# Kernel tuning notes

Measured on AMD Instinct MI355X. Metric: run time of the kernel, lower is better.

Reference implementation:

```python
import jax, jax.numpy as jnp
import numpy as np

N = 50000
E = 800000
F_IN = 128
HID = 16
HEADS = 8
C = 16
NEG_SLOPE = 0.2


def setup_inputs() -> dict:
    key = jax.random.key(0)
    ks = jax.random.split(key, 12)
    glorot = lambda k, shape: jax.random.normal(k, shape, jnp.float32) * jnp.sqrt(2.0 / (shape[0] + shape[-1]))
    return {
        "x": jax.random.normal(ks[0], (N, F_IN), jnp.float32),
        "edge_index": jax.random.randint(ks[1], (2, E), 0, N, jnp.int32),
        "x2": jax.random.normal(ks[2], (N, F_IN), jnp.float32),
        "edge_index2": jax.random.randint(ks[3], (2, E), 0, N, jnp.int32),
        # conv1: GATConv(F_IN -> HID, heads=HEADS, concat=True)
        "W1": glorot(ks[4], (F_IN, HEADS * HID)),
        "a1_src": glorot(ks[5], (HEADS, HID)),
        "a1_dst": glorot(ks[6], (HEADS, HID)),
        "b1": jnp.zeros((HEADS * HID,), jnp.float32),
        # conv2: GATConv(HEADS*HID -> C, heads=1, concat=False)
        "W2": glorot(ks[7], (HEADS * HID, 1 * C)),
        "a2_src": glorot(ks[8], (1, C)),
        "a2_dst": glorot(ks[9], (1, C)),
        "b2": jnp.zeros((C,), jnp.float32),
    }


def gat_conv(x, edge_index, W, a_src, a_dst, bias, concat):
    """PyG-style GATConv with self-loops, segment softmax over destinations."""
    n = x.shape[0]
    heads, out = a_src.shape
    h = (x @ W).reshape(n, heads, out)               # [N, H, O]
    loops = jnp.arange(n, dtype=edge_index.dtype)
    src = jnp.concatenate([edge_index[0], loops])     # messages flow src -> dst
    dst = jnp.concatenate([edge_index[1], loops])
    alpha_s = jnp.einsum('nho,ho->nh', h, a_src)
    alpha_d = jnp.einsum('nho,ho->nh', h, a_dst)
    e = jax.nn.leaky_relu(alpha_s[src] + alpha_d[dst], NEG_SLOPE)  # [E+N, H]
    m = jax.lax.stop_gradient(jax.ops.segment_max(e, dst, num_segments=n))
    w = jnp.exp(e - m[dst])
    denom = jax.ops.segment_sum(w, dst, num_segments=n)
    alpha = w / (denom[dst] + 1e-16)                  # segment softmax
    msg = h[src] * alpha[:, :, None]                  # [E+N, H, O]
    agg = jax.ops.segment_sum(msg, dst, num_segments=n)
    agg = agg.reshape(n, heads * out) if concat else agg.mean(axis=1)
    return agg + bias


def forward_once(x, edge_index, W1, a1_src, a1_dst, b1, W2, a2_src, a2_dst, b2):
    # dropout(p=0.6) is identity in eval mode
    h = jax.nn.elu(gat_conv(x, edge_index, W1, a1_src, a1_dst, b1, concat=True))
    return gat_conv(h, edge_index, W2, a2_src, a2_dst, b2, concat=False)


def reference(x, edge_index, x2, edge_index2, W1, a1_src, a1_dst, b1, W2, a2_src, a2_dst, b2):
    y = forward_once(x, edge_index, W1, a1_src, a1_dst, b1, W2, a2_src, a2_dst, b2)
    z = forward_once(x2, edge_index2, W1, a1_src, a1_dst, b1, W2, a2_src, a2_dst, b2)
    eps = 1e-8
    ny = jnp.maximum(jnp.linalg.norm(y, axis=1), eps)
    nz = jnp.maximum(jnp.linalg.norm(z, axis=1), eps)
    cos = jnp.sum(y * z, axis=1) / (ny * nz)
    ls_y = jax.nn.log_softmax(y, axis=1)
    ls_z = jax.nn.log_softmax(z, axis=1)
    return (ls_y, 1.0 - cos, ls_z, ls_y, ls_y)
```

## Files before the change

### kernel.cpp

```cpp
#include <hip/hip_runtime.h>
#include <hip/hip_bf16.h>

#define N_NODES 50000
#define N_EDGES 800000
#define F_INS   128
#define HIDDEN  16
#define HEADS   8
#define HO      128
#define C_OUT   16
#define NEG_SLOPE 0.2f
#define SLOT    64
#define NB_G1   ((N_NODES + 63) / 64)
#define NB_GAT1 ((N_NODES + 3) / 4)

#define NP      50016
#define AS_ST   ((size_t)NP * 8)
#define H1B_ST  ((size_t)NP * 64)
#define H2_ST   ((size_t)NP * 16)
#define AS2_ST  ((size_t)NP)

#define NCLS     128
#define CLS_MUL  1342u
#define CLS_SH   19
#define CAP      8192
#define CHUNK    2048
#define NB_BKT   ((N_EDGES + CHUNK - 1) / CHUNK)
#define GPAD     16

typedef unsigned short u16;
typedef unsigned int   u32;
typedef int v4i __attribute__((ext_vector_type(4)));
typedef short bf16x8 __attribute__((ext_vector_type(8)));
typedef float f32x4 __attribute__((ext_vector_type(4)));

__device__ __forceinline__ float bf2f(u16 u) {
    union { u32 i; float f; } t; t.i = ((u32)u) << 16; return t.f;
}
__device__ __forceinline__ float bflo(u32 q) {
    union { u32 i; float f; } t; t.i = q << 16; return t.f;
}
__device__ __forceinline__ float bfhi(u32 q) {
    union { u32 i; float f; } t; t.i = q & 0xFFFF0000u; return t.f;
}
__device__ __forceinline__ u32 f2bf(float f) {
    union { float f; u32 i; } t; t.f = f;
    u32 x = t.i;
    u32 lsb = (x >> 16) & 1u;
    x += 0x7FFFu + lsb;
    return x >> 16;
}
__device__ __forceinline__ u32 cvtpk(float lo, float hi) {
    u32 r;
    asm("v_cvt_pk_bf16_f32 %0, %1, %2" : "=v"(r) : "v"(lo), "v"(hi));
    return r;
}
__device__ __forceinline__ float lrelu(float t) {
    return fmaxf(t, NEG_SLOPE * t);
}
__device__ __forceinline__ int cls_of(int d) { return (int)(((u32)d * CLS_MUL) >> CLS_SH); }
__host__ __device__ __forceinline__ int cls_base(int c) { return (int)(((u32)c * 524288u + (CLS_MUL - 1)) / CLS_MUL); }

__global__ void k_wt(const float* __restrict__ W1, const float* __restrict__ a1s,
                     const float* __restrict__ a1d, const float* __restrict__ W2,
                     u32* __restrict__ w1t, u32* __restrict__ a1t,
                     float* __restrict__ w2p, int* __restrict__ gcur) {
    int t = threadIdx.x;
    if (blockIdx.x < 32) {
        int e = blockIdx.x * 256 + t;
        int c = e >> 6, kp = e & 63;
        float lo = W1[(2 * kp) * 128 + c];
        float hi = W1[(2 * kp + 1) * 128 + c];
        w1t[e] = (f2bf(hi) << 16) | f2bf(lo);
    } else {
        #pragma unroll
        for (int i = 0; i < GPAD; ++i) gcur[t * GPAD + i] = 0;
        #pragma unroll
        for (int i = 0; i < 8; ++i) {
            int idx = t * 8 + i;
            int f4 = idx >> 2, j = idx & 3;
            int sl = f4 >> 6, lane = f4 & 63;
            int s = (lane >> 4) * 8 + sl, cc = lane & 15;
            w2p[idx] = W2[(4 * s + j) * 16 + cc];
        }
        #pragma unroll
        for (int i = 0; i < 4; ++i) {
            int wi = t + i * 256;
            int n = wi >> 6, kp = wi & 63;
            int h = n >> 1;
            const float* av = ((n & 1) ? a1d : a1s) + h * 16;
            float s0 = 0.f, s1 = 0.f;
            #pragma unroll
            for (int c = 0; c < 16; ++c) {
                s0 += W1[(2 * kp) * 128 + h * 16 + c] * av[c];
                s1 += W1[(2 * kp + 1) * 128 + h * 16 + c] * av[c];
            }
            a1t[wi] = (f2bf(s1) << 16) | f2bf(s0);
        }
    }
}

__launch_bounds__(256)
__global__ void k_bg1(const int* __restrict__ ei0, const int* __restrict__ ei1,
                      int* __restrict__ gcur, u32* __restrict__ bucket,
                      const float* __restrict__ x1g, const float* __restrict__ x2g,
                      const u32* __restrict__ w1t, const u32* __restrict__ a1t,
                      u32* __restrict__ h1b, float* __restrict__ as_,
                      float* __restrict__ ad_) {
    __shared__ int cnt[NCLS];
    __shared__ int bse[NCLS];
    int t = threadIdx.x;

    if (blockIdx.x < 2 * NB_BKT) {
        int g = blockIdx.x & 1;
        int chunk = blockIdx.x >> 1;
        int e0 = chunk * CHUNK + t * 8;
        bool act = e0 < N_EDGES;

        if (t < NCLS) cnt[t] = 0;
        __syncthreads();

        const int* src = g ? ei1 : ei0;
        const int* dst = src + N_EDGES;
        int d8[8], s8[8], c8[8];
        if (act) {
            v4i da = *(const v4i*)(dst + e0), db = *(const v4i*)(dst + e0 + 4);
            v4i sa = *(const v4i*)(src + e0), sb = *(const v4i*)(src + e0 + 4);
            d8[0]=da[0]; d8[1]=da[1]; d8[2]=da[2]; d8[3]=da[3];
            d8[4]=db[0]; d8[5]=db[1]; d8[6]=db[2]; d8[7]=db[3];
            s8[0]=sa[0]; s8[1]=sa[1]; s8[2]=sa[2]; s8[3]=sa[3];
            s8[4]=sb[0]; s8[5]=sb[1]; s8[6]=sb[2]; s8[7]=sb[3];
            #pragma unroll
            for (int j = 0; j < 8; ++j) {
                c8[j] = cls_of(d8[j]);
                atomicAdd(&cnt[c8[j]], 1);
            }
        }
        __syncthreads();
        if (t < NCLS) {
            int n = cnt[t];
            bse[t] = n ? atomicAdd(&gcur[(g * NCLS + t) * GPAD], n) : 0;
            cnt[t] = 0;
        }
        __syncthreads();
        if (act) {
            #pragma unroll
            for (int j = 0; j < 8; ++j) {
                int c = c8[j];
                int p = atomicAdd(&cnt[c], 1);
                bucket[(size_t)(g * NCLS + c) * CAP + bse[c] + p] =
                    ((u32)d8[j] << 16) | (u32)s8[j];
            }
        }
        return;
    }

    int bid = blockIdx.x - 2 * NB_BKT;
    int g = bid >= NB_G1;
    if (g) bid -= NB_G1;
    const float* x = g ? x2g : x1g;
    u32*   h1o = h1b + (size_t)g * H1B_ST;
    float* aso = as_ + (size_t)g * AS_ST;
    float* ado = ad_ + (size_t)g * AS_ST;
    int r0 = bid * 64;

    int lane = t & 63;
    int wid = t >> 6;
    int n = lane & 15, quad = lane >> 4;

    int r = r0 + wid * 16 + n;
    bool rok = r < N_NODES;
    const float4* xr = (const float4*)(x + (size_t)r * 128);
    float4 xf[8];
    #pragma unroll
    for (int kt = 0; kt < 4; ++kt) {
        int cb = kt * 8 + quad * 2;
        xf[kt * 2]     = rok ? xr[cb]     : make_float4(0.f, 0.f, 0.f, 0.f);
        xf[kt * 2 + 1] = rok ? xr[cb + 1] : make_float4(0.f, 0.f, 0.f, 0.f);
    }

    f32x4 acc[8], acca;
    #pragma unroll
    for (int ct = 0; ct < 8; ++ct) acc[ct] = (f32x4){0.f, 0.f, 0.f, 0.f};
    acca = (f32x4){0.f, 0.f, 0.f, 0.f};

    #pragma unroll
    for (int kt = 0; kt < 4; ++kt) {
        union { uint4 u; bf16x8 v; } af;
        float4 f0 = xf[kt * 2], f1 = xf[kt * 2 + 1];
        af.u.x = cvtpk(f0.x, f0.y);
        af.u.y = cvtpk(f0.z, f0.w);
        af.u.z = cvtpk(f1.x, f1.y);
        af.u.w = cvtpk(f1.z, f1.w);
        #pragma unroll
        for (int ct = 0; ct < 8; ++ct) {
            union { uint4 u; bf16x8 v; } bf_;
            bf_.u = *(const uint4*)(w1t + (ct * 16 + n) * 64 + kt * 16 + quad * 4);
            acc[ct] = __builtin_amdgcn_mfma_f32_16x16x32_bf16(af.v, bf_.v, acc[ct], 0, 0, 0);
        }
        union { uint4 u; bf16x8 v; } ba;
        ba.u = *(const uint4*)(a1t + n * 64 + kt * 16 + quad * 4);
        acca = __builtin_amdgcn_mfma_f32_16x16x32_bf16(af.v, ba.v, acca, 0, 0, 0);
    }

    int h = n >> 1;
    #pragma unroll
    for (int reg = 0; reg < 4; ++reg) {
        int gr = r0 + wid * 16 + quad * 4 + reg;
        bool ok = gr <= N_NODES;
        float av = (gr == N_NODES) ? -1e30f : acca[reg];
        if (ok) {
            if (n & 1) ado[gr * 8 + h] = av;
            else       aso[gr * 8 + h] = av;
        }
        #pragma unroll
        for (int ct = 0; ct < 8; ++ct) {
            float ot = __shfl_xor(acc[ct][reg], 1);
            if (!(n & 1) && ok)
                h1o[(size_t)gr * 64 + ct * 8 + (n >> 1)] = cvtpk(acc[ct][reg], ot);
        }
    }
}

__launch_bounds__(1024)
__global__ void k_build(const int* __restrict__ gcur, const u32* __restrict__ bucket,
                        int* __restrict__ cursor, u16* __restrict__ col) {
    __shared__ int cnt[391];
    __shared__ __align__(16) u16 scol[391 * SLOT];
    int t = threadIdx.x;
    int c = blockIdx.x & (NCLS - 1);
    int g = blockIdx.x >> 7;
    int d0 = cls_base(c);
    int d1 = (c == NCLS - 1) ? N_NODES : cls_base(c + 1);
    int nn = d1 - d0;
    for (int j = t; j < nn; j += 1024) cnt[j] = 0;
    __syncthreads();

    int size = gcur[(g * NCLS + c) * GPAD];
    const u32* bp = bucket + (size_t)(g * NCLS + c) * CAP;
    for (int i = t; i < size; i += 1024) {
        u32 e = bp[i];
        int d = (int)(e >> 16);
        int s = (int)(e & 0xFFFFu);
        int p = atomicAdd(&cnt[d - d0], 1);
        if (p < SLOT) scol[(d - d0) * SLOT + p] = (u16)s;
    }
    __syncthreads();
    int* cur = cursor + g * N_NODES;
    for (int j = t; j < nn; j += 1024) {
        int raw = cnt[j];
        int n0 = min(raw, SLOT);
        int n1 = (n0 + 7) & ~7;
        for (int p = n0; p < n1; ++p) scol[j * SLOT + p] = (u16)N_NODES;
        cur[d0 + j] = raw;
    }
    __syncthreads();
    uint4* dst = (uint4*)(col + ((size_t)g * N_NODES + d0) * SLOT);
    const uint4* srcv = (const uint4*)scol;
    int n16 = nn * 8;
    for (int i = t; i < n16; i += 1024) dst[i] = srcv[i];
}

#define GAT1_ISSUE(I, qa0,qb0,qa1,qb1,qa2,qb2,qa3,qb3, A) do { \
    u32 c0_=(I).x, c1_=(I).y, c2_=(I).z, c3_=(I).w; \
    u32 i0_ = usel ? (c0_ >> 16) : (c0_ & 0xFFFFu); \
    u32 i1_ = usel ? (c1_ >> 16) : (c1_ & 0xFFFFu); \
    u32 i2_ = usel ? (c2_ >> 16) : (c2_ & 0xFFFFu); \
    u32 i3_ = usel ? (c3_ >> 16) : (c3_ & 0xFFFFu); \
    uint2 p0_ = *(const uint2*)(h1c + ((i0_ << 8) | l8)); qa0 = p0_.x; qb0 = p0_.y; \
    uint2 p1_ = *(const uint2*)(h1c + ((i1_ << 8) | l8)); qa1 = p1_.x; qb1 = p1_.y; \
    uint2 p2_ = *(const uint2*)(h1c + ((i2_ << 8) | l8)); qa2 = p2_.x; qb2 = p2_.y; \
    uint2 p3_ = *(const uint2*)(h1c + ((i3_ << 8) | l8)); qa3 = p3_.x; qb3 = p3_.y; \
    u32 ds_ = (j8 & 4) ? ((j8 & 2) ? c3_ : c2_) : ((j8 & 2) ? c1_ : c0_); \
    u32 sA_ = (j8 & 1) ? (ds_ >> 16) : (ds_ & 0xFFFFu); \
    A = *(const float*)(asc + ((sA_ << 5) | ha4)); \
} while (0)

#define GAT1_CONS(qa0,qb0,qa1,qb1,qa2,qb2,qa3,qb3, A) do { \
    int wli_ = __float_as_int(__expf(lrelu((A) + ad_a))); \
    float w0 = __int_as_float(__builtin_amdgcn_ds_bpermute(vbn,       wli_)); \
    float w1 = __int_as_float(__builtin_amdgcn_ds_bpermute(vbn + 64,  wli_)); \
    float w2 = __int_as_float(__builtin_amdgcn_ds_bpermute(vbn + 128, wli_)); \
    float w3 = __int_as_float(__builtin_amdgcn_ds_bpermute(vbn + 192, wli_)); \
    denom += ((w0 + w1) + (w2 + w3)); \
    ax0 += w0 * bflo(qa0) + w1 * bflo(qa1) + w2 * bflo(qa2) + w3 * bflo(qa3); \
    ax1 += w0 * bfhi(qa0) + w1 * bfhi(qa1) + w2 * bfhi(qa2) + w3 * bfhi(qa3); \
    ax2 += w0 * bflo(qb0) + w1 * bflo(qb1) + w2 * bflo(qb2) + w3 * bflo(qb3); \
    ax3 += w0 * bfhi(qb0) + w1 * bfhi(qb1) + w2 * bfhi(qb2) + w3 * bfhi(qb3); \
} while (0)

__launch_bounds__(256)
__global__ void k_gat1f(const u32* __restrict__ h1b, const float* __restrict__ as_,
                        const float* __restrict__ ad_, const int* __restrict__ cursor,
                        const u16* __restrict__ col, const float* __restrict__ b1,
                        const float* __restrict__ w2p, const float* __restrict__ a2s,
                        const float* __restrict__ a2d, float* __restrict__ h2,
                        float* __restrict__ as2, float* __restrict__ ad2) {
    int t = threadIdx.x;
    int lane = t & 63;
    int bid = blockIdx.x;
    if (bid == 2 * NB_GAT1) {
        if (t < 32) {
            int g = t >> 4, c = t & 15;
            h2[(size_t)g * H2_ST + (size_t)N_NODES * 16 + c] = 0.f;
            if (c == 0) {
                as2[(size_t)g * AS2_ST + N_NODES] = -1e30f;
                ad2[(size_t)g * AS2_ST + N_NODES] = 0.f;
            }
        }
        return;
    }
    int g = bid >= NB_GAT1;
    if (g) bid -= NB_GAT1;
    int node = bid * 4 + (t >> 6);

    const char*  h1c = (const char*)(h1b + (size_t)g * H1B_ST);
    const char*  asc = (const char*)(as_ + (size_t)g * AS_ST);
    const float* ad1 = ad_ + (size_t)g * AS_ST;
    const u16*   cp  = col + ((size_t)g * N_NODES + node) * SLOT;
    float* h2o  = h2  + (size_t)g * H2_ST;
    float* as2o = as2 + (size_t)g * AS2_ST;
    float* ad2o = ad2 + (size_t)g * AS2_ST;

    int l = lane & 31;
    int usel = lane >> 5;
    u32 l8 = (u32)l << 3;
    int hc = l >> 2;
    int ha = lane & 7;
    int j8 = lane >> 3;
    u32 ha4 = (u32)ha << 2;
    int vbn = usel * 32 + hc * 4;

    float ad_a = ad1[node * 8 + ha];
    float as_c = as_[(size_t)g * AS_ST + node * 8 + hc];
    float ad_c = ad1[node * 8 + hc];

    float w = __expf(lrelu(as_c + ad_c));
    float ws = usel ? 0.f : w;
    uint2 sq = *(const uint2*)(h1c + (((u32)node << 8) | l8));
    float denom = ws;
    float ax0 = ws * bflo(sq.x), ax1 = ws * bfhi(sq.x);
    float ax2 = ws * bflo(sq.y), ax3 = ws * bfhi(sq.y);

    int deg = min(cursor[g * N_NODES + node], SLOT);
    int nb = (deg + 7) >> 3;
    if (nb) {
        u32 a0,b0,a1,b1_,a2,b2,a3,b3;
        u32 c0,d0,c1,d1,c2,d2,c3,d3;
        float Aa, Ab;
        uint4 Ia, Ib;
        Ia = *(const uint4*)cp;
        GAT1_ISSUE(Ia, a0,b0,a1,b1_,a2,b2,a3,b3, Aa);
        if (nb > 1) {
            Ib = *(const uint4*)(cp + 8);
            GAT1_ISSUE(Ib, c0,d0,c1,d1,c2,d2,c3,d3, Ab);
        }
        int b = 0;
        for (;;) {
            GAT1_CONS(a0,b0,a1,b1_,a2,b2,a3,b3, Aa);
            if (++b >= nb) break;
            if (b + 1 < nb) {
                Ia = *(const uint4*)(cp + (b + 1) * 8);
                GAT1_ISSUE(Ia, a0,b0,a1,b1_,a2,b2,a3,b3, Aa);
            }
            GAT1_CONS(c0,d0,c1,d1,c2,d2,c3,d3, Ab);
            if (++b >= nb) break;
            if (b + 1 < nb) {
                Ib = *(const uint4*)(cp + (b + 1) * 8);
                GAT1_ISSUE(Ib, c0,d0,c1,d1,c2,d2,c3,d3, Ab);
            }
        }
    }
    denom += __shfl_xor(denom, 32);
    ax0 += __shfl_xor(ax0, 32);
    ax1 += __shfl_xor(ax1, 32);
    ax2 += __shfl_xor(ax2, 32);
    ax3 += __shfl_xor(ax3, 32);

    float inv = 1.f / (denom + 1e-16f);
    int cb = l * 4;
    float o0 = ax0 * inv + b1[cb];
    float o1 = ax1 * inv + b1[cb + 1];
    float o2 = ax2 * inv + b1[cb + 2];
    float o3 = ax3 * inv + b1[cb + 3];
    o0 = (o0 > 0.f) ? o0 : (__expf(o0) - 1.f);
    o1 = (o1 > 0.f) ? o1 : (__expf(o1) - 1.f);
    o2 = (o2 > 0.f) ? o2 : (__expf(o2) - 1.f);
    o3 = (o3 > 0.f) ? o3 : (__expf(o3) - 1.f);
    u32 q2a = cvtpk(o0, o1);
    u32 q2b = cvtpk(o2, o3);

    int cc = lane & 15, seg = lane >> 4;
    const float4* wr = (const float4*)w2p;
    float acc2 = 0.f;
    #pragma unroll
    for (int sl = 0; sl < 8; ++sl) {
        float4 wv = wr[sl * 64 + lane];
        int sb = (seg * 8 + sl) << 2;
        u32 va = (u32)__builtin_amdgcn_ds_bpermute(sb, (int)q2a);
        u32 vb = (u32)__builtin_amdgcn_ds_bpermute(sb, (int)q2b);
        acc2 += bflo(va) * wv.x + bfhi(va) * wv.y
              + bflo(vb) * wv.z + bfhi(vb) * wv.w;
    }
    acc2 += __shfl_xor(acc2, 16);
    acc2 += __shfl_xor(acc2, 32);
    if (lane < 16) h2o[(u32)node * 16 + cc] = acc2;

    float sa = acc2 * a2s[cc];
    float sd = acc2 * a2d[cc];
    #pragma unroll
    for (int m = 1; m < 16; m <<= 1) {
        sa += __shfl_xor(sa, m);
        sd += __shfl_xor(sd, m);
    }
    if (lane == 0) { as2o[node] = sa; ad2o[node] = sd; }
}

#define G2_ISSUE(I, H2C, ASC, v0,v1,v2,v3,v4,v5,v6,v7, A) do { \
    u32 ix_=(I).x, iy_=(I).y, iz_=(I).z, iw_=(I).w; \
    v0 = *(const float*)((H2C) + (((ix_ & 0xFFFFu) << 6) | c4)); \
    v1 = *(const float*)((H2C) + (((ix_ >> 16)     << 6) | c4)); \
    v2 = *(const float*)((H2C) + (((iy_ & 0xFFFFu) << 6) | c4)); \
    v3 = *(const float*)((H2C) + (((iy_ >> 16)     << 6) | c4)); \
    v4 = *(const float*)((H2C) + (((iz_ & 0xFFFFu) << 6) | c4)); \
    v5 = *(const float*)((H2C) + (((iz_ >> 16)     << 6) | c4)); \
    v6 = *(const float*)((H2C) + (((iw_ & 0xFFFFu) << 6) | c4)); \
    v7 = *(const float*)((H2C) + (((iw_ >> 16)     << 6) | c4)); \
    u32 ds_ = (jsel & 4) ? ((jsel & 2) ? iw_ : iz_) : ((jsel & 2) ? iy_ : ix_); \
    u32 sA_ = (jsel & 1) ? (ds_ >> 16) : (ds_ & 0xFFFFu); \
    A = *(const float*)((ASC) + (sA_ << 2)); \
} while (0)

#define G2_CONS(v0,v1,v2,v3,v4,v5,v6,v7, A, AD, DEN, ACC) do { \
    int wli_ = __float_as_int(__expf(lrelu((A) + (AD)))); \
    float w0 = __int_as_float(__builtin_amdgcn_ds_bpermute(gb,      wli_)); \
    float w1 = __int_as_float(__builtin_amdgcn_ds_bpermute(gb + 4,  wli_)); \
    float w2 = __int_as_float(__builtin_amdgcn_ds_bpermute(gb + 8,  wli_)); \
    float w3 = __int_as_float(__builtin_amdgcn_ds_bpermute(gb + 12, wli_)); \
    float w4 = __int_as_float(__builtin_amdgcn_ds_bpermute(gb + 16, wli_)); \
    float w5 = __int_as_float(__builtin_amdgcn_ds_bpermute(gb + 20, wli_)); \
    float w6 = __int_as_float(__builtin_amdgcn_ds_bpermute(gb + 24, wli_)); \
    float w7 = __int_as_float(__builtin_amdgcn_ds_bpermute(gb + 28, wli_)); \
    DEN += ((w0 + w1) + (w2 + w3)) + ((w4 + w5) + (w6 + w7)); \
    ACC += (w0 * v0 + w1 * v1 + w2 * v2 + w3 * v3) \
         + (w4 * v4 + w5 * v5 + w6 * v6 + w7 * v7); \
} while (0)

__launch_bounds__(256)
__global__ void k_gat2e(const float* __restrict__ h2, const float* __restrict__ as2,
                        const float* __restrict__ ad2, const int* __restrict__ cursor,
                        const u16* __restrict__ col, const float* __restrict__ b2,
                        float* __restrict__ out) {
    int t = threadIdx.x;
    int node = blockIdx.x * 16 + (t >> 4);
    int c = t & 15;
    int lane = t & 63;
    u32 c4 = (u32)c << 2;
    int jsel = lane & 7;
    u32 gb = (u32)(lane & 48) << 2;
    float b2c = b2[c];

    const char* h2Y = (const char*)h2;
    const char* h2Z = (const char*)(h2 + H2_ST);
    const char* asY = (const char*)as2;
    const char* asZ = (const char*)(as2 + AS2_ST);
    const u16* cpY = col + (size_t)node * SLOT;
    const u16* cpZ = col + ((size_t)N_NODES + node) * SLOT;
    float adY = ad2[node];
    float adZ = ad2[AS2_ST + node];

    float wY = __expf(lrelu(*(const float*)(asY + ((u32)node << 2)) + adY));
    float dY = wY;
    float aY = wY * *(const float*)(h2Y + (((u32)node << 6) | c4));
    float wZ = __expf(lrelu(*(const float*)(asZ + ((u32)node << 2)) + adZ));
    float dZ = wZ;
    float aZ = wZ * *(const float*)(h2Z + (((u32)node << 6) | c4));

    int nbY = (min(cursor[node], SLOT) + 7) >> 3;
    int nbZ = (min(cursor[N_NODES + node], SLOT) + 7) >> 3;

    float y0,y1,y2,y3,y4,y5,y6,y7, Ay;
    float z0,z1,z2,z3,z4,z5,z6,z7, Az;
    uint4 I;
    if (nbY) { I = *(const uint4*)cpY; G2_ISSUE(I, h2Y, asY, y0,y1,y2,y3,y4,y5,y6,y7, Ay); }
    if (nbZ) { I = *(const uint4*)cpZ; G2_ISSUE(I, h2Z, asZ, z0,z1,z2,z3,z4,z5,z6,z7, Az); }
    int bY = 0, bZ = 0;
    while (bY < nbY || bZ < nbZ) {
        if (bY < nbY) {
            G2_CONS(y0,y1,y2,y3,y4,y5,y6,y7, Ay, adY, dY, aY);
            ++bY;
            if (bY < nbY) {
                I = *(const uint4*)(cpY + bY * 8);
                G2_ISSUE(I, h2Y, asY, y0,y1,y2,y3,y4,y5,y6,y7, Ay);
            }
        }
        if (bZ < nbZ) {
            G2_CONS(z0,z1,z2,z3,z4,z5,z6,z7, Az, adZ, dZ, aZ);
            ++bZ;
            if (bZ < nbZ) {
                I = *(const uint4*)(cpZ + bZ * 8);
                G2_ISSUE(I, h2Z, asZ, z0,z1,z2,z3,z4,z5,z6,z7, Az);
            }
        }
    }
    float yv = aY / (dY + 1e-16f) + b2c;
    float zv = aZ / (dZ + 1e-16f) + b2c;

    float my = yv, mz = zv;
    #pragma unroll
    for (int m = 1; m < 16; m <<= 1) {
        my = fmaxf(my, __shfl_xor(my, m));
        mz = fmaxf(mz, __shfl_xor(mz, m));
    }
    float sy = __expf(yv - my), sz = __expf(zv - mz);
    float dot = yv * zv, ny = yv * yv, nz = zv * zv;
    #pragma unroll
    for (int m = 1; m < 16; m <<= 1) {
        sy  += __shfl_xor(sy, m);
        sz  += __shfl_xor(sz, m);
        dot += __shfl_xor(dot, m);
        ny  += __shfl_xor(ny, m);
        nz  += __shfl_xor(nz, m);
    }
    float lsey = my + __logf(sy);
    float lsez = mz + __logf(sz);
    float omc = 1.f - dot / (fmaxf(sqrtf(ny), 1e-8f) * fmaxf(sqrtf(nz), 1e-8f));

    const int O1 = N_NODES * C_OUT;
    const int O2 = O1 + N_NODES;
    const int O3 = O2 + N_NODES * C_OUT;
    const int O4 = O3 + N_NODES * C_OUT;
    float ly = yv - lsey;
    float lz = zv - lsez;
    int base = node * 16 + c;
    out[base]      = ly;
    out[O2 + base] = lz;
    out[O3 + base] = ly;
    out[O4 + base] = ly;
    if (c == 0) out[O1 + node] = omc;
}

extern "C" void kernel_launch(void* const* d_in, const int* in_sizes, int n_in,
                              void* d_out, int out_size, void* d_ws, size_t ws_size,
                              hipStream_t stream) {
    (void)in_sizes; (void)n_in; (void)out_size; (void)ws_size;
    const float* x1  = (const float*)d_in[0];
    const int*   ei1 = (const int*)d_in[1];
    const float* x2  = (const float*)d_in[2];
    const int*   ei2 = (const int*)d_in[3];
    const float* W1  = (const float*)d_in[4];
    const float* a1s = (const float*)d_in[5];
    const float* a1d = (const float*)d_in[6];
    const float* b1  = (const float*)d_in[7];
    const float* W2  = (const float*)d_in[8];
    const float* a2s = (const float*)d_in[9];
    const float* a2d = (const float*)d_in[10];
    const float* b2  = (const float*)d_in[11];
    float* out = (float*)d_out;

    char* p = (char*)d_ws;
    int* gcur      = (int*)p; p += (size_t)2 * NCLS * GPAD * 4;
    u32* w1t       = (u32*)p; p += (size_t)128 * 64 * 4;
    u32* a1t       = (u32*)p; p += (size_t)16 * 64 * 4;
    float* w2p     = (float*)p; p += (size_t)16 * 128 * 4;
    int* cursor    = (int*)p; p += (size_t)2 * N_NODES * 4;
    u16* col       = (u16*)p; p += (size_t)2 * N_NODES * SLOT * 2;
    float* as1  = (float*)p; p += (size_t)2 * AS_ST * 4;
    float* ad1  = (float*)p; p += (size_t)2 * AS_ST * 4;
    float* h2   = (float*)p; p += (size_t)2 * H2_ST * 4;
    float* as2  = (float*)p; p += (size_t)2 * AS2_ST * 4;
    float* ad2  = (float*)p; p += (size_t)2 * AS2_ST * 4;
    u32* bucket = (u32*)p;   p += (size_t)2 * NCLS * CAP * 4;
    u32* h1b    = (u32*)p;   p += (size_t)2 * H1B_ST * 4;

    k_wt    <<<33, 256, 0, stream>>>(W1, a1s, a1d, W2, w1t, a1t, w2p, gcur);
    k_bg1   <<<2 * NB_BKT + 2 * NB_G1, 256, 0, stream>>>(ei1, ei2, gcur, bucket,
                                                         x1, x2, w1t, a1t, h1b, as1, ad1);
    k_build <<<2 * NCLS, 1024, 0, stream>>>(gcur, bucket, cursor, col);
    k_gat1f <<<2 * NB_GAT1 + 1, 256, 0, stream>>>(h1b, as1, ad1, cursor, col, b1,
                                                  w2p, a2s, a2d, h2, as2, ad2);
    k_gat2e <<<N_NODES / 16, 256, 0, stream>>>(h2, as2, ad2, cursor, col, b2, out);
}
```

Before: 279.5 us.

## Process two nodes per wavefront in GAT layer-1 with cross-node gather prefetch

Each wavefront in the fused layer-1 aggregation kernel now handles two consecutive destination nodes instead of one, halving the grid size. The first gather batches for the second node are issued before the first node's W2 projection and reductions, so those loads can overlap that epilogue math. This targets exposed gather latency and per-wave setup overhead, at the cost of higher register pressure and less parallelism, which may reduce occupancy.

```diff
diff --git a/kernel.cpp b/kernel.cpp
--- a/kernel.cpp
+++ b/kernel.cpp
@@ -11,7 +11,7 @@
 #define NEG_SLOPE 0.2f
 #define SLOT    64
 #define NB_G1   ((N_NODES + 63) / 64)
-#define NB_GAT1 ((N_NODES + 3) / 4)
+#define NB_GAT1P ((N_NODES + 7) / 8)
 
 #define NP      50016
 #define AS_ST   ((size_t)NP * 8)
@@ -288,6 +288,24 @@
     ax3 += w0 * bfhi(qb0) + w1 * bfhi(qb1) + w2 * bfhi(qb2) + w3 * bfhi(qb3); \
 } while (0)
 
+#define GAT1_LOOP(CP, NB) do { \
+    int b_ = 0; \
+    for (;;) { \
+        GAT1_CONS(a0,b0,a1,b1_,a2,b2,a3,b3, Aa); \
+        if (++b_ >= (NB)) break; \
+        if (b_ + 1 < (NB)) { \
+            I4 = *(const uint4*)((CP) + (b_ + 1) * 8); \
+            GAT1_ISSUE(I4, a0,b0,a1,b1_,a2,b2,a3,b3, Aa); \
+        } \
+        GAT1_CONS(c0,d0,c1,d1,c2,d2,c3,d3, Ab); \
+        if (++b_ >= (NB)) break; \
+        if (b_ + 1 < (NB)) { \
+            I4 = *(const uint4*)((CP) + (b_ + 1) * 8); \
+            GAT1_ISSUE(I4, c0,d0,c1,d1,c2,d2,c3,d3, Ab); \
+        } \
+    } \
+} while (0)
+
 __launch_bounds__(256)
 __global__ void k_gat1f(const u32* __restrict__ h1b, const float* __restrict__ as_,
                         const float* __restrict__ ad_, const int* __restrict__ cursor,
@@ -298,7 +316,7 @@
     int t = threadIdx.x;
     int lane = t & 63;
     int bid = blockIdx.x;
-    if (bid == 2 * NB_GAT1) {
+    if (bid == 2 * NB_GAT1P) {
         if (t < 32) {
             int g = t >> 4, c = t & 15;
             h2[(size_t)g * H2_ST + (size_t)N_NODES * 16 + c] = 0.f;
@@ -309,14 +327,16 @@
         }
         return;
     }
-    int g = bid >= NB_GAT1;
-    if (g) bid -= NB_GAT1;
-    int node = bid * 4 + (t >> 6);
+    int g = bid >= NB_GAT1P;
+    if (g) bid -= NB_GAT1P;
+    int nodeA = bid * 8 + (t >> 6) * 2;
+    int nodeB = nodeA + 1;
 
     const char*  h1c = (const char*)(h1b + (size_t)g * H1B_ST);
     const char*  asc = (const char*)(as_ + (size_t)g * AS_ST);
     const float* ad1 = ad_ + (size_t)g * AS_ST;
-    const u16*   cp  = col + ((size_t)g * N_NODES + node) * SLOT;
+    const u16*   cpA = col + ((size_t)g * N_NODES + nodeA) * SLOT;
+    const u16*   cpB = cpA + SLOT;
     float* h2o  = h2  + (size_t)g * H2_ST;
     float* as2o = as2 + (size_t)g * AS2_ST;
     float* ad2o = ad2 + (size_t)g * AS2_ST;
@@ -329,55 +349,41 @@
     int j8 = lane >> 3;
     u32 ha4 = (u32)ha << 2;
     int vbn = usel * 32 + hc * 4;
-
-    float ad_a = ad1[node * 8 + ha];
-    float as_c = as_[(size_t)g * AS_ST + node * 8 + hc];
-    float ad_c = ad1[node * 8 + hc];
-
-    float w = __expf(lrelu(as_c + ad_c));
-    float ws = usel ? 0.f : w;
-    uint2 sq = *(const uint2*)(h1c + (((u32)node << 8) | l8));
-    float denom = ws;
-    float ax0 = ws * bflo(sq.x), ax1 = ws * bfhi(sq.x);
-    float ax2 = ws * bflo(sq.y), ax3 = ws * bfhi(sq.y);
-
-    int deg = min(cursor[g * N_NODES + node], SLOT);
-    int nb = (deg + 7) >> 3;
-    if (nb) {
-        u32 a0,b0,a1,b1_,a2,b2,a3,b3;
-        u32 c0,d0,c1,d1,c2,d2,c3,d3;
-        float Aa, Ab;
-        uint4 Ia, Ib;
-        Ia = *(const uint4*)cp;
-        GAT1_ISSUE(Ia, a0,b0,a1,b1_,a2,b2,a3,b3, Aa);
-        if (nb > 1) {
-            Ib = *(const uint4*)(cp + 8);
-            GAT1_ISSUE(Ib, c0,d0,c1,d1,c2,d2,c3,d3, Ab);
-        }
-        int b = 0;
-        for (;;) {
-            GAT1_CONS(a0,b0,a1,b1_,a2,b2,a3,b3, Aa);
-            if (++b >= nb) break;
-            if (b + 1 < nb) {
-                Ia = *(const uint4*)(cp + (b + 1) * 8);
-                GAT1_ISSUE(Ia, a0,b0,a1,b1_,a2,b2,a3,b3, Aa);
-            }
-            GAT1_CONS(c0,d0,c1,d1,c2,d2,c3,d3, Ab);
-            if (++b >= nb) break;
-            if (b + 1 < nb) {
-                Ib = *(const uint4*)(cp + (b + 1) * 8);
-                GAT1_ISSUE(Ib, c0,d0,c1,d1,c2,d2,c3,d3, Ab);
-            }
-        }
+    int cb = l * 4;
+    int cc = lane & 15, seg = lane >> 4;
+    const float4* wr = (const float4*)w2p;
+
+    u32 a0,b0,a1,b1_,a2,b2,a3,b3;
+    u32 c0,d0,c1,d1,c2,d2,c3,d3;
+    float Aa, Ab;
+    uint4 I4;
+
+    float ad_a = ad1[nodeA * 8 + ha];
+    float as_cA = as_[(size_t)g * AS_ST + nodeA * 8 + hc];
+    float ad_cA = ad1[nodeA * 8 + hc];
+    float wsA = usel ? 0.f : __expf(lrelu(as_cA + ad_cA));
+    uint2 sq = *(const uint2*)(h1c + (((u32)nodeA << 8) | l8));
+    float denom = wsA;
+    float ax0 = wsA * bflo(sq.x), ax1 = wsA * bfhi(sq.x);
+    float ax2 = wsA * bflo(sq.y), ax3 = wsA * bfhi(sq.y);
+
+    int nbA = (min(cursor[g * N_NODES + nodeA], SLOT) + 7) >> 3;
+    int nbB = (min(cursor[g * N_NODES + nodeB], SLOT) + 7) >> 3;
+    if (nbA) {
+        I4 = *(const uint4*)cpA;
+        GAT1_ISSUE(I4, a0,b0,a1,b1_,a2,b2,a3,b3, Aa);
+        if (nbA > 1) {
+            I4 = *(const uint4*)(cpA + 8);
+            GAT1_ISSUE(I4, c0,d0,c1,d1,c2,d2,c3,d3, Ab);
+        }
+        GAT1_LOOP(cpA, nbA);
     }
     denom += __shfl_xor(denom, 32);
     ax0 += __shfl_xor(ax0, 32);
     ax1 += __shfl_xor(ax1, 32);
     ax2 += __shfl_xor(ax2, 32);
     ax3 += __shfl_xor(ax3, 32);
-
     float inv = 1.f / (denom + 1e-16f);
-    int cb = l * 4;
     float o0 = ax0 * inv + b1[cb];
     float o1 = ax1 * inv + b1[cb + 1];
     float o2 = ax2 * inv + b1[cb + 2];
@@ -389,8 +395,19 @@
     u32 q2a = cvtpk(o0, o1);
     u32 q2b = cvtpk(o2, o3);
 
-    int cc = lane & 15, seg = lane >> 4;
-    const float4* wr = (const float4*)w2p;
+    float ad_aB = ad1[nodeB * 8 + ha];
+    float as_cB = as_[(size_t)g * AS_ST + nodeB * 8 + hc];
+    float ad_cB = ad1[nodeB * 8 + hc];
+    uint2 sqB = *(const uint2*)(h1c + (((u32)nodeB << 8) | l8));
+    if (nbB) {
+        I4 = *(const uint4*)cpB;
+        GAT1_ISSUE(I4, a0,b0,a1,b1_,a2,b2,a3,b3, Aa);
+        if (nbB > 1) {
+            I4 = *(const uint4*)(cpB + 8);
+            GAT1_ISSUE(I4, c0,d0,c1,d1,c2,d2,c3,d3, Ab);
+        }
+    }
+
     float acc2 = 0.f;
     #pragma unroll
     for (int sl = 0; sl < 8; ++sl) {
@@ -403,8 +420,7 @@
     }
     acc2 += __shfl_xor(acc2, 16);
     acc2 += __shfl_xor(acc2, 32);
-    if (lane < 16) h2o[(u32)node * 16 + cc] = acc2;
-
+    if (lane < 16) h2o[(u32)nodeA * 16 + cc] = acc2;
     float sa = acc2 * a2s[cc];
     float sd = acc2 * a2d[cc];
     #pragma unroll
@@ -412,7 +428,52 @@
         sa += __shfl_xor(sa, m);
         sd += __shfl_xor(sd, m);
     }
-    if (lane == 0) { as2o[node] = sa; ad2o[node] = sd; }
+    if (lane == 0) { as2o[nodeA] = sa; ad2o[nodeA] = sd; }
+
+    ad_a = ad_aB;
+    float wsB = usel ? 0.f : __expf(lrelu(as_cB + ad_cB));
+    denom = wsB;
+    ax0 = wsB * bflo(sqB.x); ax1 = wsB * bfhi(sqB.x);
+    ax2 = wsB * bflo(sqB.y); ax3 = wsB * bfhi(sqB.y);
+    if (nbB) GAT1_LOOP(cpB, nbB);
+    denom += __shfl_xor(denom, 32);
+    ax0 += __shfl_xor(ax0, 32);
+    ax1 += __shfl_xor(ax1, 32);
+    ax2 += __shfl_xor(ax2, 32);
+    ax3 += __shfl_xor(ax3, 32);
+    inv = 1.f / (denom + 1e-16f);
+    o0 = ax0 * inv + b1[cb];
+    o1 = ax1 * inv + b1[cb + 1];
+    o2 = ax2 * inv + b1[cb + 2];
+    o3 = ax3 * inv + b1[cb + 3];
+    o0 = (o0 > 0.f) ? o0 : (__expf(o0) - 1.f);
+    o1 = (o1 > 0.f) ? o1 : (__expf(o1) - 1.f);
+    o2 = (o2 > 0.f) ? o2 : (__expf(o2) - 1.f);
+    o3 = (o3 > 0.f) ? o3 : (__expf(o3) - 1.f);
+    q2a = cvtpk(o0, o1);
+    q2b = cvtpk(o2, o3);
+
+    acc2 = 0.f;
+    #pragma unroll
+    for (int sl = 0; sl < 8; ++sl) {
+        float4 wv = wr[sl * 64 + lane];
+        int sb = (seg * 8 + sl) << 2;
+        u32 va = (u32)__builtin_amdgcn_ds_bpermute(sb, (int)q2a);
+        u32 vb = (u32)__builtin_amdgcn_ds_bpermute(sb, (int)q2b);
+        acc2 += bflo(va) * wv.x + bfhi(va) * wv.y
+              + bflo(vb) * wv.z + bfhi(vb) * wv.w;
+    }
+    acc2 += __shfl_xor(acc2, 16);
+    acc2 += __shfl_xor(acc2, 32);
+    if (lane < 16) h2o[(u32)nodeB * 16 + cc] = acc2;
+    sa = acc2 * a2s[cc];
+    sd = acc2 * a2d[cc];
+    #pragma unroll
+    for (int m = 1; m < 16; m <<= 1) {
+        sa += __shfl_xor(sa, m);
+        sd += __shfl_xor(sd, m);
+    }
+    if (lane == 0) { as2o[nodeB] = sa; ad2o[nodeB] = sd; }
 }
 
 #define G2_ISSUE(I, H2C, ASC, v0,v1,v2,v3,v4,v5,v6,v7, A) do { \
@@ -576,7 +637,7 @@
     k_bg1   <<<2 * NB_BKT + 2 * NB_G1, 256, 0, stream>>>(ei1, ei2, gcur, bucket,
                                                          x1, x2, w1t, a1t, h1b, as1, ad1);
     k_build <<<2 * NCLS, 1024, 0, stream>>>(gcur, bucket, cursor, col);
-    k_gat1f <<<2 * NB_GAT1 + 1, 256, 0, stream>>>(h1b, as1, ad1, cursor, col, b1,
-                                                  w2p, a2s, a2d, h2, as2, ad2);
+    k_gat1f <<<2 * NB_GAT1P + 1, 256, 0, stream>>>(h1b, as1, ad1, cursor, col, b1,
+                                                   w2p, a2s, a2d, h2, as2, ad2);
     k_gat2e <<<N_NODES / 16, 256, 0, stream>>>(h2, as2, ad2, cursor, col, b2, out);
 }
```

After: 307.5 us. +10.0%, slower.
